# Kernel tuning notes

Hardware: AMD Instinct MI355X
Metric: run time of the kernel (lower is better)

## Reference

```python
import jax, jax.numpy as jnp
import numpy as np

N, E = 20000, 320000
DIMS = [(200, 64), (64, 128), (128, 256), (256, 256), (256, 512)]


def _embed(v):
    # NeRF positional encoding, multires=10, include_input, log-sampled freqs, [sin, cos] per freq
    freqs = 2.0 ** jnp.arange(10, dtype=jnp.float32)
    ang = v[:, None, :] * freqs[None, :, None]           # [N, 10, 3]
    sc = jnp.stack([jnp.sin(ang), jnp.cos(ang)], 2)      # [N, 10, 2, 3] (freq-major, sin then cos)
    return jnp.concatenate([v, sc.reshape(v.shape[0], -1)], -1)  # [N, 63]


def _edge_conv(h, src, dst, w1, b1, w2, b2):
    # PyG EdgeConv: nn([x_i, x_j - x_i]) aggregated by mean onto target i
    hi = h[dst]
    hj = h[src]
    m = jnp.concatenate([hi, hj - hi], -1)               # [E, 2*in]
    m = jax.nn.relu(m @ w1 + b1) @ w2 + b2               # [E, out]
    s = jax.ops.segment_sum(m, dst, num_segments=N)
    cnt = jax.ops.segment_sum(jnp.ones((m.shape[0], 1), m.dtype), dst, num_segments=N)
    return s / jnp.maximum(cnt, 1.0)                     # scatter-mean (0 for isolated nodes)


def _bn(h, g, b):
    # training-mode BatchNorm1d over nodes (biased variance, eps=1e-5)
    mu = h.mean(0)
    var = ((h - mu) ** 2).mean(0)
    return g * (h - mu) * jax.lax.rsqrt(var + 1e-5) + b


def setup_inputs() -> dict:
    key = jax.random.key(0)
    keys = iter(jax.random.split(key, 64))
    inp = {
        "x": jax.random.normal(next(keys), (N, 20), jnp.float32),
        "edge_index": jax.random.randint(next(keys), (2, E), 0, N, jnp.int32),
        "batch": jnp.zeros((N,), jnp.int32),
    }
    for i, (din, dout) in enumerate(DIMS, 1):
        inp[f"gc{i}_w1"] = jax.random.normal(next(keys), (2 * din, dout), jnp.float32) / np.sqrt(2.0 * din)
        inp[f"gc{i}_b1"] = jnp.zeros((dout,), jnp.float32)
        inp[f"gc{i}_w2"] = jax.random.normal(next(keys), (dout, dout), jnp.float32) / np.sqrt(1.0 * dout)
        inp[f"gc{i}_b2"] = jnp.zeros((dout,), jnp.float32)
    for i, d in enumerate([64, 128, 256, 256], 1):
        inp[f"n{i}_g"] = jnp.ones((d,), jnp.float32)
        inp[f"n{i}_b"] = jnp.zeros((d,), jnp.float32)
    return inp


def reference(x, edge_index, batch,
              gc1_w1, gc1_b1, gc1_w2, gc1_b2,
              gc2_w1, gc2_b1, gc2_w2, gc2_b2,
              gc3_w1, gc3_b1, gc3_w2, gc3_b2,
              gc4_w1, gc4_b1, gc4_w2, gc4_b2,
              gc5_w1, gc5_b1, gc5_w2, gc5_b2,
              n1_g, n1_b, n2_g, n2_b, n3_g, n3_b, n4_g, n4_b):
    src, dst = edge_index[0], edge_index[1]
    h = jnp.concatenate(
        [_embed(x[:, 0:3]), _embed(x[:, 3:6]), _embed(x[:, 6:9]), x[:, 9:20]], -1)  # [N, 200]
    h = jax.nn.relu(_bn(_edge_conv(h, src, dst, gc1_w1, gc1_b1, gc1_w2, gc1_b2), n1_g, n1_b))
    h = jax.nn.relu(_bn(_edge_conv(h, src, dst, gc2_w1, gc2_b1, gc2_w2, gc2_b2), n2_g, n2_b))
    h = jax.nn.relu(_bn(_edge_conv(h, src, dst, gc3_w1, gc3_b1, gc3_w2, gc3_b2), n3_g, n3_b))
    h = jax.nn.relu(_bn(_edge_conv(h, src, dst, gc4_w1, gc4_b1, gc4_w2, gc4_b2), n4_g, n4_b))
    return _edge_conv(h, src, dst, gc5_w1, gc5_b1, gc5_w2, gc5_b2)  # [N, 512]
```

## Files before the change

### kernel.cpp

```cpp
#include <hip/hip_runtime.h>
#include <math.h>

#define NNODES 20000
#define NEDGES 320000
#define NB 79

typedef __bf16 bf16x8 __attribute__((ext_vector_type(8)));
typedef float f32x4 __attribute__((ext_vector_type(4)));
typedef unsigned short u16x8 __attribute__((ext_vector_type(8)));

__device__ inline unsigned short f2bf(float x) {
  union { float f; unsigned int u; } q;
  q.f = x;
  unsigned int u = q.u;
  unsigned int r = (u + 0x7fffu + ((u >> 16) & 1u)) >> 16;
  return (unsigned short)r;
}

__device__ inline float bf2f(unsigned short u) {
  union { unsigned int u; float f; } q;
  q.u = ((unsigned int)u) << 16;
  return q.f;
}

__global__ __launch_bounds__(256) void embed_kernel(const float* __restrict__ x,
                                                    unsigned short* __restrict__ h) {
  int n = blockIdx.x * blockDim.x + threadIdx.x;
  if (n >= NNODES) return;
  const float* xr = x + (size_t)n * 20;
  unsigned short* hr = h + (size_t)n * 224;
#pragma unroll
  for (int g = 0; g < 3; ++g) {
    float v0 = xr[g * 3 + 0], v1 = xr[g * 3 + 1], v2 = xr[g * 3 + 2];
    unsigned short* o = hr + g * 63;
    o[0] = f2bf(v0); o[1] = f2bf(v1); o[2] = f2bf(v2);
    float f = 1.0f;
    for (int fr = 0; fr < 10; ++fr) {
      float s0, c0, s1, c1, s2, c2;
      sincosf(v0 * f, &s0, &c0);
      sincosf(v1 * f, &s1, &c1);
      sincosf(v2 * f, &s2, &c2);
      int base = 3 + fr * 6;
      o[base + 0] = f2bf(s0); o[base + 1] = f2bf(s1); o[base + 2] = f2bf(s2);
      o[base + 3] = f2bf(c0); o[base + 4] = f2bf(c1); o[base + 5] = f2bf(c2);
      f *= 2.0f;
    }
  }
  for (int j = 0; j < 11; ++j) hr[189 + j] = f2bf(xr[9 + j]);
  for (int j = 200; j < 224; ++j) hr[j] = 0;
}

__global__ __launch_bounds__(256) void count_kernel(const int* __restrict__ edst,
                                                    int* __restrict__ cnt) {
  int e = blockIdx.x * blockDim.x + threadIdx.x;
  if (e < NEDGES) atomicAdd(&cnt[edst[e]], 1);
}

__global__ __launch_bounds__(256) void scan_pass1(const int* __restrict__ cnt,
                                                  int* __restrict__ bsum) {
  __shared__ int red[256];
  int i = blockIdx.x * 256 + threadIdx.x;
  int v = (i < NNODES) ? cnt[i] : 0;
  red[threadIdx.x] = v;
  __syncthreads();
#pragma unroll
  for (int off = 128; off > 0; off >>= 1) {
    if (threadIdx.x < off) red[threadIdx.x] += red[threadIdx.x + off];
    __syncthreads();
  }
  if (threadIdx.x == 0) bsum[blockIdx.x] = red[0];
}

__global__ __launch_bounds__(128) void scan_pass2(const int* __restrict__ bsum,
                                                  int* __restrict__ boff) {
  __shared__ int buf[128];
  int t = threadIdx.x;
  int v = (t < NB) ? bsum[t] : 0;
  buf[t] = v;
  __syncthreads();
#pragma unroll
  for (int off = 1; off < 128; off <<= 1) {
    int u = (t >= off) ? buf[t - off] : 0;
    __syncthreads();
    buf[t] += u;
    __syncthreads();
  }
  if (t < NB) boff[t] = buf[t] - v;
}

__global__ __launch_bounds__(256) void scan_pass3(const int* __restrict__ cnt,
                                                  const int* __restrict__ boff,
                                                  int* __restrict__ rowptr,
                                                  int* __restrict__ head) {
  __shared__ int buf[256];
  int i = blockIdx.x * 256 + threadIdx.x;
  int v = (i < NNODES) ? cnt[i] : 0;
  buf[threadIdx.x] = v;
  __syncthreads();
#pragma unroll
  for (int off = 1; off < 256; off <<= 1) {
    int u = (threadIdx.x >= off) ? buf[threadIdx.x - off] : 0;
    __syncthreads();
    buf[threadIdx.x] += u;
    __syncthreads();
  }
  if (i < NNODES) {
    int excl = boff[blockIdx.x] + buf[threadIdx.x] - v;
    rowptr[i] = excl;
    head[i] = excl;
  }
  if (i == 0) rowptr[NNODES] = NEDGES;
}

__global__ __launch_bounds__(256) void scatter_kernel(const int* __restrict__ esrc,
                                                      const int* __restrict__ edst,
                                                      int* __restrict__ head,
                                                      int* __restrict__ csr_src) {
  int e = blockIdx.x * blockDim.x + threadIdx.x;
  if (e < NEDGES) {
    int pos = atomicAdd(&head[edst[e]], 1);
    csr_src[pos] = esrc[e];
  }
}

struct WPtrs {
  const float* w1[5];
  const float* w2[5];
};

#define WT1_TOTAL 503808
#define WT2_TOTAL 413696

__global__ __launch_bounds__(256) void weight_prep_kernel(
    WPtrs p, unsigned short* __restrict__ Wt1All,
    unsigned short* __restrict__ Wt2All) {
  int idx = blockIdx.x * 256 + threadIdx.x;
  if (idx < WT1_TOTAL) {
    int L, off, din, dout, Kpad;
    if (idx < 28672)       { L = 0; off = 0;      din = 200; dout = 64;  Kpad = 224; }
    else if (idx < 45056)  { L = 1; off = 28672;  din = 64;  dout = 128; Kpad = 64;  }
    else if (idx < 110592) { L = 2; off = 45056;  din = 128; dout = 256; Kpad = 128; }
    else if (idx < 241664) { L = 3; off = 110592; din = 256; dout = 256; Kpad = 256; }
    else                   { L = 4; off = 241664; din = 256; dout = 512; Kpad = 256; }
    int local = idx - off;
    int c = local / Kpad, k = local % Kpad;
    float v = 0.f;
    if (k < din)
      v = (c < dout) ? p.w1[L][(size_t)k * dout + c]
                     : p.w1[L][(size_t)(din + k) * dout + (c - dout)];
    Wt1All[idx] = f2bf(v);
    return;
  }
  int jdx = idx - WT1_TOTAL;
  if (jdx >= WT2_TOTAL) return;
  int L, off, d;
  if (jdx < 4096)        { L = 0; off = 0;      d = 64;  }
  else if (jdx < 20480)  { L = 1; off = 4096;   d = 128; }
  else if (jdx < 86016)  { L = 2; off = 20480;  d = 256; }
  else if (jdx < 151552) { L = 3; off = 86016;  d = 256; }
  else                   { L = 4; off = 151552; d = 512; }
  int local = jdx - off;
  int n = local / d, k = local % d;
  Wt2All[jdx] = f2bf(p.w2[L][(size_t)k * d + n]);
}

template <int EPI>
__global__ __launch_bounds__(256) void mfma_gemm_kernel(
    const unsigned short* __restrict__ A, int lda, int K,
    const unsigned short* __restrict__ Bt, int Ncol, int dhalf,
    const float* __restrict__ bias, const int* __restrict__ cnt,
    float* __restrict__ stats, void* __restrict__ Cout) {
  __shared__ unsigned short sA[128 * 40];
  __shared__ unsigned short sB[64 * 40];
  int tid = threadIdx.x;
  int bR = blockIdx.y * 128, bC = blockIdx.x * 64;
  int wid = tid >> 6, lane = tid & 63;
  int wr = wid >> 1, wc = wid & 1;
  int lr = lane & 15, lg = lane >> 4;

  f32x4 acc[4][2];
#pragma unroll
  for (int fr = 0; fr < 4; ++fr)
#pragma unroll
    for (int fc = 0; fc < 2; ++fc) acc[fr][fc] = f32x4{0.f, 0.f, 0.f, 0.f};

  for (int k0 = 0; k0 < K; k0 += 32) {
#pragma unroll
    for (int rep = 0; rep < 2; ++rep) {
      int idx = tid + rep * 256;
      int row = idx >> 2, kq = (idx & 3) * 8;
      int gr = bR + row;
      bf16x8 v;
      if (gr < NNODES) {
        v = *(const bf16x8*)(A + (size_t)gr * lda + k0 + kq);
      } else {
#pragma unroll
        for (int i = 0; i < 8; ++i) v[i] = (__bf16)0.f;
      }
      *(bf16x8*)(sA + row * 40 + kq) = v;
    }
    {
      int n = tid >> 2, kq = (tid & 3) * 8;
      bf16x8 v = *(const bf16x8*)(Bt + (size_t)(bC + n) * K + k0 + kq);
      *(bf16x8*)(sB + n * 40 + kq) = v;
    }
    __syncthreads();
    bf16x8 aF[4], bF[2];
#pragma unroll
    for (int fr = 0; fr < 4; ++fr)
      aF[fr] = *(const bf16x8*)(sA + (wr * 64 + fr * 16 + lr) * 40 + lg * 8);
#pragma unroll
    for (int fc = 0; fc < 2; ++fc)
      bF[fc] = *(const bf16x8*)(sB + (wc * 32 + fc * 16 + lr) * 40 + lg * 8);
#pragma unroll
    for (int fr = 0; fr < 4; ++fr)
#pragma unroll
      for (int fc = 0; fc < 2; ++fc)
        acc[fr][fc] = __builtin_amdgcn_mfma_f32_16x16x32_bf16(
            aF[fr], bF[fc], acc[fr][fc], 0, 0, 0);
    __syncthreads();
  }

  float csum[2] = {0.f, 0.f}, csum2[2] = {0.f, 0.f};
#pragma unroll
  for (int fr = 0; fr < 4; ++fr) {
#pragma unroll
    for (int j = 0; j < 4; ++j) {
      int gr = bR + wr * 64 + fr * 16 + lg * 4 + j;
      if (gr >= NNODES) continue;
      int ct = (EPI >= 1) ? cnt[gr] : 1;
#pragma unroll
      for (int fc = 0; fc < 2; ++fc) {
        int gc = bC + wc * 32 + fc * 16 + lr;
        float v = acc[fr][fc][j];
        if (EPI == 0) {
          if (gc < dhalf) v += bias[gc];
          ((unsigned short*)Cout)[(size_t)gr * Ncol + gc] = f2bf(v);
        } else {
          v = (ct > 0) ? (v + bias[gc]) : 0.f;
          ((float*)Cout)[(size_t)gr * Ncol + gc] = v;
          if (EPI == 2) {
            csum[fc] += v;
            csum2[fc] += v * v;
          }
        }
      }
    }
  }
  if (EPI == 2) {
#pragma unroll
    for (int fc = 0; fc < 2; ++fc) {
      float s = csum[fc], s2 = csum2[fc];
      s += __shfl_xor(s, 16, 64);
      s += __shfl_xor(s, 32, 64);
      s2 += __shfl_xor(s2, 16, 64);
      s2 += __shfl_xor(s2, 32, 64);
      if (lg == 0) {
        int gc = bC + wc * 32 + fc * 16 + lr;
        atomicAdd(&stats[gc], s);
        atomicAdd(&stats[Ncol + gc], s2);
      }
    }
  }
}

template <int D, int SLICES>
__global__ __launch_bounds__(256) void edge_agg_kernel(
    const unsigned short* __restrict__ AV, const int* __restrict__ rowptr,
    const int* __restrict__ csr_src, unsigned short* __restrict__ Y) {
  int slice = blockIdx.x % SLICES;
  int ngrp = blockIdx.x / SLICES;
  int tid = threadIdx.x;
  int ln = tid & 7;
  int sn = tid >> 3;
  int node = ngrp * 32 + sn;
  if (node >= NNODES) return;
  int c = slice * 64 + ln * 8;
  const unsigned short* Arow = AV + (size_t)node * 2 * D;
  u16x8 a8 = *(const u16x8*)(Arow + c);
  u16x8 v8 = *(const u16x8*)(Arow + D + c);
  float ad[8], acc[8];
#pragma unroll
  for (int i = 0; i < 8; ++i) {
    ad[i] = bf2f(a8[i]) - bf2f(v8[i]);
    acc[i] = 0.f;
  }
  int e0 = rowptr[node], e1 = rowptr[node + 1];
  int e = e0;
  for (; e + 3 < e1; e += 4) {
    int s0 = csr_src[e], s1 = csr_src[e + 1];
    int s2 = csr_src[e + 2], s3 = csr_src[e + 3];
    u16x8 w0 = *(const u16x8*)(AV + (size_t)s0 * 2 * D + D + c);
    u16x8 w1 = *(const u16x8*)(AV + (size_t)s1 * 2 * D + D + c);
    u16x8 w2 = *(const u16x8*)(AV + (size_t)s2 * 2 * D + D + c);
    u16x8 w3 = *(const u16x8*)(AV + (size_t)s3 * 2 * D + D + c);
#pragma unroll
    for (int i = 0; i < 8; ++i) {
      acc[i] += fmaxf(ad[i] + bf2f(w0[i]), 0.f) + fmaxf(ad[i] + bf2f(w1[i]), 0.f) +
                fmaxf(ad[i] + bf2f(w2[i]), 0.f) + fmaxf(ad[i] + bf2f(w3[i]), 0.f);
    }
  }
  for (; e < e1; ++e) {
    int s0 = csr_src[e];
    u16x8 w0 = *(const u16x8*)(AV + (size_t)s0 * 2 * D + D + c);
#pragma unroll
    for (int i = 0; i < 8; ++i) acc[i] += fmaxf(ad[i] + bf2f(w0[i]), 0.f);
  }
  float inv = (e1 > e0) ? 1.f / (float)(e1 - e0) : 0.f;
  u16x8 o;
#pragma unroll
  for (int i = 0; i < 8; ++i) o[i] = f2bf(acc[i] * inv);
  *(u16x8*)(Y + (size_t)node * D + c) = o;
}

__global__ __launch_bounds__(256) void bn_relu_kernel(
    const float* __restrict__ S, const float* __restrict__ stats,
    const float* __restrict__ g, const float* __restrict__ bb, int dout,
    unsigned short* __restrict__ Hout) {
  size_t idx = (size_t)blockIdx.x * blockDim.x + threadIdx.x;
  size_t total = (size_t)NNODES * dout;
  if (idx >= total) return;
  int c = (int)(idx % dout);
  float mu = stats[c] * (1.0f / NNODES);
  float var = stats[dout + c] * (1.0f / NNODES) - mu * mu;
  float y = S[idx];
  float v = g[c] * (y - mu) * rsqrtf(var + 1e-5f) + bb[c];
  Hout[idx] = f2bf(fmaxf(v, 0.f));
}

static void launch_edge_agg(int dout, const unsigned short* AV, const int* rowptr,
                            const int* csr_src, unsigned short* Y,
                            hipStream_t st) {
  const int NG = (NNODES + 31) / 32;
  switch (dout) {
    case 64:
      hipLaunchKernelGGL((edge_agg_kernel<64, 1>), dim3(NG * 1), dim3(256), 0, st,
                         AV, rowptr, csr_src, Y);
      break;
    case 128:
      hipLaunchKernelGGL((edge_agg_kernel<128, 2>), dim3(NG * 2), dim3(256), 0, st,
                         AV, rowptr, csr_src, Y);
      break;
    case 256:
      hipLaunchKernelGGL((edge_agg_kernel<256, 4>), dim3(NG * 4), dim3(256), 0, st,
                         AV, rowptr, csr_src, Y);
      break;
    case 512:
      hipLaunchKernelGGL((edge_agg_kernel<512, 8>), dim3(NG * 8), dim3(256), 0, st,
                         AV, rowptr, csr_src, Y);
      break;
  }
}

extern "C" void kernel_launch(void* const* d_in, const int* in_sizes, int n_in,
                              void* d_out, int out_size, void* d_ws,
                              size_t ws_size, hipStream_t stream) {
  const float* x = (const float*)d_in[0];
  const int* edge_index = (const int*)d_in[1];
  const int* esrc = edge_index;
  const int* edst = edge_index + NEDGES;

  const float* gw1[5] = {(const float*)d_in[3],  (const float*)d_in[7],
                         (const float*)d_in[11], (const float*)d_in[15],
                         (const float*)d_in[19]};
  const float* gb1[5] = {(const float*)d_in[4],  (const float*)d_in[8],
                         (const float*)d_in[12], (const float*)d_in[16],
                         (const float*)d_in[20]};
  const float* gw2[5] = {(const float*)d_in[5],  (const float*)d_in[9],
                         (const float*)d_in[13], (const float*)d_in[17],
                         (const float*)d_in[21]};
  const float* gb2[5] = {(const float*)d_in[6],  (const float*)d_in[10],
                         (const float*)d_in[14], (const float*)d_in[18],
                         (const float*)d_in[22]};
  const float* ng[4] = {(const float*)d_in[23], (const float*)d_in[25],
                        (const float*)d_in[27], (const float*)d_in[29]};
  const float* nb[4] = {(const float*)d_in[24], (const float*)d_in[26],
                        (const float*)d_in[28], (const float*)d_in[30]};

  unsigned short* AV = (unsigned short*)d_ws;
  float* S = (float*)(AV + (size_t)NNODES * 1024);
  unsigned short* Hbf = (unsigned short*)(S + (size_t)NNODES * 256);
  unsigned short* Ybf = Hbf + (size_t)NNODES * 256;
  unsigned short* Wt1All = Ybf + (size_t)NNODES * 512;
  unsigned short* Wt2All = Wt1All + WT1_TOTAL;
  int* cnt = (int*)(Wt2All + WT2_TOTAL);
  int* rowptr = cnt + NNODES;
  int* head = rowptr + NNODES + 1;
  int* csr_src = head + NNODES;
  int* bsum = csr_src + NEDGES;
  int* boff = bsum + NB;
  float* stats = (float*)(boff + NB);

  const int Kpads[5] = {224, 64, 128, 256, 256};
  const int douts[5] = {64, 128, 256, 256, 512};
  const int wt1_off[5] = {0, 28672, 45056, 110592, 241664};
  const int wt2_off[5] = {0, 4096, 20480, 86016, 151552};
  const int MBLK = (NNODES + 127) / 128;

  hipMemsetAsync(cnt, 0, NNODES * sizeof(int), stream);
  hipMemsetAsync(stats, 0, 4 * 1024 * sizeof(float), stream);
  count_kernel<<<(NEDGES + 255) / 256, 256, 0, stream>>>(edst, cnt);
  scan_pass1<<<NB, 256, 0, stream>>>(cnt, bsum);
  scan_pass2<<<1, 128, 0, stream>>>(bsum, boff);
  scan_pass3<<<NB, 256, 0, stream>>>(cnt, boff, rowptr, head);
  scatter_kernel<<<(NEDGES + 255) / 256, 256, 0, stream>>>(esrc, edst, head, csr_src);
  embed_kernel<<<(NNODES + 255) / 256, 256, 0, stream>>>(x, Hbf);

  WPtrs wp;
  for (int i = 0; i < 5; ++i) { wp.w1[i] = gw1[i]; wp.w2[i] = gw2[i]; }
  weight_prep_kernel<<<(WT1_TOTAL + WT2_TOTAL + 255) / 256, 256, 0, stream>>>(
      wp, Wt1All, Wt2All);

  int lda = 224;
  for (int L = 0; L < 5; ++L) {
    int Kp = Kpads[L], dout = douts[L];
    dim3 g1(2 * dout / 64, MBLK);
    hipLaunchKernelGGL((mfma_gemm_kernel<0>), g1, dim3(256), 0, stream,
                       Hbf, lda, Kp, Wt1All + wt1_off[L], 2 * dout, dout, gb1[L],
                       (const int*)nullptr, (float*)nullptr, (void*)AV);
    launch_edge_agg(dout, AV, rowptr, csr_src, Ybf, stream);
    dim3 g2(dout / 64, MBLK);
    if (L < 4) {
      float* lstats = stats + L * 1024;
      hipLaunchKernelGGL((mfma_gemm_kernel<2>), g2, dim3(256), 0, stream,
                         Ybf, dout, dout, Wt2All + wt2_off[L], dout, dout, gb2[L],
                         cnt, lstats, (void*)S);
      size_t total = (size_t)NNODES * dout;
      bn_relu_kernel<<<(total + 255) / 256, 256, 0, stream>>>(
          S, lstats, ng[L], nb[L], dout, Hbf);
      lda = dout;
    } else {
      hipLaunchKernelGGL((mfma_gemm_kernel<1>), g2, dim3(256), 0, stream,
                         Ybf, dout, dout, Wt2All + wt2_off[L], dout, dout, gb2[L],
                         cnt, (float*)nullptr, (void*)d_out);
    }
  }
}
```

Measured before the change: 461.7 us.

## Fuse BatchNorm+ReLU into next GEMM prologue and enlarge GEMM tiles to 128x128

The standalone bn_relu kernel is removed. The next layer's first GEMM now reads the fp32 pre-BN activations, builds per-channel scale and shift from the accumulated stats, and applies normalize+ReLU while loading the A tile into shared memory. The GEMM tile grows from 128x64 with K-step 32 to 128x128 with K-step 64, and layer-1 input padding goes from 224 to 256 so K divides the tile. This saves one full read/write pass of the hidden state per layer and improves reuse per block, at the cost of reading fp32 instead of bf16 A operands and fewer blocks in the grid.

```diff
diff --git a/kernel.cpp b/kernel.cpp
--- a/kernel.cpp
+++ b/kernel.cpp
@@ -28,7 +28,7 @@
   int n = blockIdx.x * blockDim.x + threadIdx.x;
   if (n >= NNODES) return;
   const float* xr = x + (size_t)n * 20;
-  unsigned short* hr = h + (size_t)n * 224;
+  unsigned short* hr = h + (size_t)n * 256;
 #pragma unroll
   for (int g = 0; g < 3; ++g) {
     float v0 = xr[g * 3 + 0], v1 = xr[g * 3 + 1], v2 = xr[g * 3 + 2];
@@ -47,7 +47,7 @@
     }
   }
   for (int j = 0; j < 11; ++j) hr[189 + j] = f2bf(xr[9 + j]);
-  for (int j = 200; j < 224; ++j) hr[j] = 0;
+  for (int j = 200; j < 256; ++j) hr[j] = 0;
 }
 
 __global__ __launch_bounds__(256) void count_kernel(const int* __restrict__ edst,
@@ -128,7 +128,7 @@
   const float* w2[5];
 };
 
-#define WT1_TOTAL 503808
+#define WT1_TOTAL 507904
 #define WT2_TOTAL 413696
 
 __global__ __launch_bounds__(256) void weight_prep_kernel(
@@ -137,11 +137,11 @@
   int idx = blockIdx.x * 256 + threadIdx.x;
   if (idx < WT1_TOTAL) {
     int L, off, din, dout, Kpad;
-    if (idx < 28672)       { L = 0; off = 0;      din = 200; dout = 64;  Kpad = 224; }
-    else if (idx < 45056)  { L = 1; off = 28672;  din = 64;  dout = 128; Kpad = 64;  }
-    else if (idx < 110592) { L = 2; off = 45056;  din = 128; dout = 256; Kpad = 128; }
-    else if (idx < 241664) { L = 3; off = 110592; din = 256; dout = 256; Kpad = 256; }
-    else                   { L = 4; off = 241664; din = 256; dout = 512; Kpad = 256; }
+    if (idx < 32768)       { L = 0; off = 0;      din = 200; dout = 64;  Kpad = 256; }
+    else if (idx < 49152)  { L = 1; off = 32768;  din = 64;  dout = 128; Kpad = 64;  }
+    else if (idx < 114688) { L = 2; off = 49152;  din = 128; dout = 256; Kpad = 128; }
+    else if (idx < 245760) { L = 3; off = 114688; din = 256; dout = 256; Kpad = 256; }
+    else                   { L = 4; off = 245760; din = 256; dout = 512; Kpad = 256; }
     int local = idx - off;
     int c = local / Kpad, k = local % Kpad;
     float v = 0.f;
@@ -164,64 +164,103 @@
   Wt2All[jdx] = f2bf(p.w2[L][(size_t)k * d + n]);
 }
 
-template <int EPI>
-__global__ __launch_bounds__(256) void mfma_gemm_kernel(
-    const unsigned short* __restrict__ A, int lda, int K,
+template <int EPI, int EPIA>
+__global__ __launch_bounds__(256) void gemm128_kernel(
+    const void* __restrict__ Aptr, int lda, int K,
     const unsigned short* __restrict__ Bt, int Ncol, int dhalf,
     const float* __restrict__ bias, const int* __restrict__ cnt,
-    float* __restrict__ stats, void* __restrict__ Cout) {
-  __shared__ unsigned short sA[128 * 40];
-  __shared__ unsigned short sB[64 * 40];
+    const float* __restrict__ pstats, const float* __restrict__ pg,
+    const float* __restrict__ pb, float* __restrict__ stats,
+    void* __restrict__ Cout) {
+  __shared__ unsigned short sA[128 * 72];
+  __shared__ unsigned short sB[128 * 72];
+  __shared__ float sScale[256], sShift[256];
   int tid = threadIdx.x;
-  int bR = blockIdx.y * 128, bC = blockIdx.x * 64;
+  int bR = blockIdx.y * 128, bC = blockIdx.x * 128;
   int wid = tid >> 6, lane = tid & 63;
   int wr = wid >> 1, wc = wid & 1;
   int lr = lane & 15, lg = lane >> 4;
 
-  f32x4 acc[4][2];
+  if (EPIA == 1) {
+    for (int c = tid; c < K; c += 256) {
+      float mu = pstats[c] * (1.0f / NNODES);
+      float var = pstats[K + c] * (1.0f / NNODES) - mu * mu;
+      float sc = pg[c] * rsqrtf(var + 1e-5f);
+      sScale[c] = sc;
+      sShift[c] = pb[c] - mu * sc;
+    }
+    __syncthreads();
+  }
+
+  f32x4 acc[4][4];
 #pragma unroll
   for (int fr = 0; fr < 4; ++fr)
 #pragma unroll
-    for (int fc = 0; fc < 2; ++fc) acc[fr][fc] = f32x4{0.f, 0.f, 0.f, 0.f};
-
-  for (int k0 = 0; k0 < K; k0 += 32) {
-#pragma unroll
-    for (int rep = 0; rep < 2; ++rep) {
-      int idx = tid + rep * 256;
-      int row = idx >> 2, kq = (idx & 3) * 8;
+    for (int fc = 0; fc < 4; ++fc) acc[fr][fc] = f32x4{0.f, 0.f, 0.f, 0.f};
+
+  for (int k0 = 0; k0 < K; k0 += 64) {
+#pragma unroll
+    for (int i = 0; i < 4; ++i) {
+      int idx = tid + i * 256;
+      int row = idx >> 3, c8 = (idx & 7) * 8;
       int gr = bR + row;
-      bf16x8 v;
-      if (gr < NNODES) {
-        v = *(const bf16x8*)(A + (size_t)gr * lda + k0 + kq);
+      if (EPIA == 0) {
+        bf16x8 v;
+        if (gr < NNODES) {
+          v = *(const bf16x8*)((const unsigned short*)Aptr + (size_t)gr * lda + k0 + c8);
+        } else {
+#pragma unroll
+          for (int j = 0; j < 8; ++j) v[j] = (__bf16)0.f;
+        }
+        *(bf16x8*)(sA + row * 72 + c8) = v;
       } else {
-#pragma unroll
-        for (int i = 0; i < 8; ++i) v[i] = (__bf16)0.f;
+        const float* Af = (const float*)Aptr;
+        float uv[8];
+#pragma unroll
+        for (int j = 0; j < 8; ++j) uv[j] = 0.f;
+        if (gr < NNODES) {
+          float4 u0 = *(const float4*)(Af + (size_t)gr * lda + k0 + c8);
+          float4 u1 = *(const float4*)(Af + (size_t)gr * lda + k0 + c8 + 4);
+          uv[0] = u0.x; uv[1] = u0.y; uv[2] = u0.z; uv[3] = u0.w;
+          uv[4] = u1.x; uv[5] = u1.y; uv[6] = u1.z; uv[7] = u1.w;
+        }
+        u16x8 o;
+#pragma unroll
+        for (int j = 0; j < 8; ++j) {
+          int k = k0 + c8 + j;
+          o[j] = f2bf(fmaxf(uv[j] * sScale[k] + sShift[k], 0.f));
+        }
+        *(u16x8*)(sA + row * 72 + c8) = o;
       }
-      *(bf16x8*)(sA + row * 40 + kq) = v;
-    }
-    {
-      int n = tid >> 2, kq = (tid & 3) * 8;
-      bf16x8 v = *(const bf16x8*)(Bt + (size_t)(bC + n) * K + k0 + kq);
-      *(bf16x8*)(sB + n * 40 + kq) = v;
-    }
-    __syncthreads();
-    bf16x8 aF[4], bF[2];
-#pragma unroll
-    for (int fr = 0; fr < 4; ++fr)
-      aF[fr] = *(const bf16x8*)(sA + (wr * 64 + fr * 16 + lr) * 40 + lg * 8);
-#pragma unroll
-    for (int fc = 0; fc < 2; ++fc)
-      bF[fc] = *(const bf16x8*)(sB + (wc * 32 + fc * 16 + lr) * 40 + lg * 8);
-#pragma unroll
-    for (int fr = 0; fr < 4; ++fr)
-#pragma unroll
-      for (int fc = 0; fc < 2; ++fc)
-        acc[fr][fc] = __builtin_amdgcn_mfma_f32_16x16x32_bf16(
-            aF[fr], bF[fc], acc[fr][fc], 0, 0, 0);
-    __syncthreads();
-  }
-
-  float csum[2] = {0.f, 0.f}, csum2[2] = {0.f, 0.f};
+    }
+#pragma unroll
+    for (int i = 0; i < 4; ++i) {
+      int idx = tid + i * 256;
+      int n = idx >> 3, c8 = (idx & 7) * 8;
+      bf16x8 v = *(const bf16x8*)(Bt + (size_t)(bC + n) * K + k0 + c8);
+      *(bf16x8*)(sB + n * 72 + c8) = v;
+    }
+    __syncthreads();
+#pragma unroll
+    for (int ks = 0; ks < 2; ++ks) {
+      bf16x8 aF[4], bF[4];
+#pragma unroll
+      for (int fr = 0; fr < 4; ++fr)
+        aF[fr] = *(const bf16x8*)(sA + (wr * 64 + fr * 16 + lr) * 72 + ks * 32 + lg * 8);
+#pragma unroll
+      for (int fc = 0; fc < 4; ++fc)
+        bF[fc] = *(const bf16x8*)(sB + (wc * 64 + fc * 16 + lr) * 72 + ks * 32 + lg * 8);
+#pragma unroll
+      for (int fr = 0; fr < 4; ++fr)
+#pragma unroll
+        for (int fc = 0; fc < 4; ++fc)
+          acc[fr][fc] = __builtin_amdgcn_mfma_f32_16x16x32_bf16(
+              aF[fr], bF[fc], acc[fr][fc], 0, 0, 0);
+    }
+    __syncthreads();
+  }
+
+  float csum[4] = {0.f, 0.f, 0.f, 0.f}, csum2[4] = {0.f, 0.f, 0.f, 0.f};
 #pragma unroll
   for (int fr = 0; fr < 4; ++fr) {
 #pragma unroll
@@ -230,8 +269,8 @@
       if (gr >= NNODES) continue;
       int ct = (EPI >= 1) ? cnt[gr] : 1;
 #pragma unroll
-      for (int fc = 0; fc < 2; ++fc) {
-        int gc = bC + wc * 32 + fc * 16 + lr;
+      for (int fc = 0; fc < 4; ++fc) {
+        int gc = bC + wc * 64 + fc * 16 + lr;
         float v = acc[fr][fc][j];
         if (EPI == 0) {
           if (gc < dhalf) v += bias[gc];
@@ -249,17 +288,107 @@
   }
   if (EPI == 2) {
 #pragma unroll
-    for (int fc = 0; fc < 2; ++fc) {
+    for (int fc = 0; fc < 4; ++fc) {
       float s = csum[fc], s2 = csum2[fc];
       s += __shfl_xor(s, 16, 64);
       s += __shfl_xor(s, 32, 64);
       s2 += __shfl_xor(s2, 16, 64);
       s2 += __shfl_xor(s2, 32, 64);
       if (lg == 0) {
-        int gc = bC + wc * 32 + fc * 16 + lr;
+        int gc = bC + wc * 64 + fc * 16 + lr;
         atomicAdd(&stats[gc], s);
         atomicAdd(&stats[Ncol + gc], s2);
       }
+    }
+  }
+}
+
+__global__ __launch_bounds__(256) void gemm64_stats_kernel(
+    const unsigned short* __restrict__ A, int lda, int K,
+    const unsigned short* __restrict__ Bt, int Ncol,
+    const float* __restrict__ bias, const int* __restrict__ cnt,
+    float* __restrict__ stats, float* __restrict__ Cout) {
+  __shared__ unsigned short sA[128 * 40];
+  __shared__ unsigned short sB[64 * 40];
+  int tid = threadIdx.x;
+  int bR = blockIdx.y * 128, bC = blockIdx.x * 64;
+  int wid = tid >> 6, lane = tid & 63;
+  int wr = wid >> 1, wc = wid & 1;
+  int lr = lane & 15, lg = lane >> 4;
+
+  f32x4 acc[4][2];
+#pragma unroll
+  for (int fr = 0; fr < 4; ++fr)
+#pragma unroll
+    for (int fc = 0; fc < 2; ++fc) acc[fr][fc] = f32x4{0.f, 0.f, 0.f, 0.f};
+
+  for (int k0 = 0; k0 < K; k0 += 32) {
+#pragma unroll
+    for (int rep = 0; rep < 2; ++rep) {
+      int idx = tid + rep * 256;
+      int row = idx >> 2, kq = (idx & 3) * 8;
+      int gr = bR + row;
+      bf16x8 v;
+      if (gr < NNODES) {
+        v = *(const bf16x8*)(A + (size_t)gr * lda + k0 + kq);
+      } else {
+#pragma unroll
+        for (int i = 0; i < 8; ++i) v[i] = (__bf16)0.f;
+      }
+      *(bf16x8*)(sA + row * 40 + kq) = v;
+    }
+    {
+      int n = tid >> 2, kq = (tid & 3) * 8;
+      bf16x8 v = *(const bf16x8*)(Bt + (size_t)(bC + n) * K + k0 + kq);
+      *(bf16x8*)(sB + n * 40 + kq) = v;
+    }
+    __syncthreads();
+    bf16x8 aF[4], bF[2];
+#pragma unroll
+    for (int fr = 0; fr < 4; ++fr)
+      aF[fr] = *(const bf16x8*)(sA + (wr * 64 + fr * 16 + lr) * 40 + lg * 8);
+#pragma unroll
+    for (int fc = 0; fc < 2; ++fc)
+      bF[fc] = *(const bf16x8*)(sB + (wc * 32 + fc * 16 + lr) * 40 + lg * 8);
+#pragma unroll
+    for (int fr = 0; fr < 4; ++fr)
+#pragma unroll
+      for (int fc = 0; fc < 2; ++fc)
+        acc[fr][fc] = __builtin_amdgcn_mfma_f32_16x16x32_bf16(
+            aF[fr], bF[fc], acc[fr][fc], 0, 0, 0);
+    __syncthreads();
+  }
+
+  float csum[2] = {0.f, 0.f}, csum2[2] = {0.f, 0.f};
+#pragma unroll
+  for (int fr = 0; fr < 4; ++fr) {
+#pragma unroll
+    for (int j = 0; j < 4; ++j) {
+      int gr = bR + wr * 64 + fr * 16 + lg * 4 + j;
+      if (gr >= NNODES) continue;
+      int ct = cnt[gr];
+#pragma unroll
+      for (int fc = 0; fc < 2; ++fc) {
+        int gc = bC + wc * 32 + fc * 16 + lr;
+        float v = acc[fr][fc][j];
+        v = (ct > 0) ? (v + bias[gc]) : 0.f;
+        Cout[(size_t)gr * Ncol + gc] = v;
+        csum[fc] += v;
+        csum2[fc] += v * v;
+      }
+    }
+  }
+#pragma unroll
+  for (int fc = 0; fc < 2; ++fc) {
+    float s = csum[fc], s2 = csum2[fc];
+    s += __shfl_xor(s, 16, 64);
+    s += __shfl_xor(s, 32, 64);
+    s2 += __shfl_xor(s2, 16, 64);
+    s2 += __shfl_xor(s2, 32, 64);
+    if (lg == 0) {
+      int gc = bC + wc * 32 + fc * 16 + lr;
+      atomicAdd(&stats[gc], s);
+      atomicAdd(&stats[Ncol + gc], s2);
     }
   }
 }
@@ -311,21 +440,6 @@
 #pragma unroll
   for (int i = 0; i < 8; ++i) o[i] = f2bf(acc[i] * inv);
   *(u16x8*)(Y + (size_t)node * D + c) = o;
-}
-
-__global__ __launch_bounds__(256) void bn_relu_kernel(
-    const float* __restrict__ S, const float* __restrict__ stats,
-    const float* __restrict__ g, const float* __restrict__ bb, int dout,
-    unsigned short* __restrict__ Hout) {
-  size_t idx = (size_t)blockIdx.x * blockDim.x + threadIdx.x;
-  size_t total = (size_t)NNODES * dout;
-  if (idx >= total) return;
-  int c = (int)(idx % dout);
-  float mu = stats[c] * (1.0f / NNODES);
-  float var = stats[dout + c] * (1.0f / NNODES) - mu * mu;
-  float y = S[idx];
-  float v = g[c] * (y - mu) * rsqrtf(var + 1e-5f) + bb[c];
-  Hout[idx] = f2bf(fmaxf(v, 0.f));
 }
 
 static void launch_edge_agg(int dout, const unsigned short* AV, const int* rowptr,
@@ -391,9 +505,9 @@
   int* boff = bsum + NB;
   float* stats = (float*)(boff + NB);
 
-  const int Kpads[5] = {224, 64, 128, 256, 256};
+  const int Kpads[5] = {256, 64, 128, 256, 256};
   const int douts[5] = {64, 128, 256, 256, 512};
-  const int wt1_off[5] = {0, 28672, 45056, 110592, 241664};
+  const int wt1_off[5] = {0, 32768, 49152, 114688, 245760};
   const int wt2_off[5] = {0, 4096, 20480, 86016, 151552};
   const int MBLK = (NNODES + 127) / 128;
 
@@ -411,28 +525,42 @@
   weight_prep_kernel<<<(WT1_TOTAL + WT2_TOTAL + 255) / 256, 256, 0, stream>>>(
       wp, Wt1All, Wt2All);
 
-  int lda = 224;
   for (int L = 0; L < 5; ++L) {
     int Kp = Kpads[L], dout = douts[L];
-    dim3 g1(2 * dout / 64, MBLK);
-    hipLaunchKernelGGL((mfma_gemm_kernel<0>), g1, dim3(256), 0, stream,
-                       Hbf, lda, Kp, Wt1All + wt1_off[L], 2 * dout, dout, gb1[L],
-                       (const int*)nullptr, (float*)nullptr, (void*)AV);
+    dim3 g1(2 * dout / 128, MBLK);
+    if (L == 0) {
+      hipLaunchKernelGGL((gemm128_kernel<0, 0>), g1, dim3(256), 0, stream,
+                         (const void*)Hbf, 256, Kp, Wt1All + wt1_off[L], 2 * dout,
+                         dout, gb1[L], (const int*)nullptr, (const float*)nullptr,
+                         (const float*)nullptr, (const float*)nullptr,
+                         (float*)nullptr, (void*)AV);
+    } else {
+      hipLaunchKernelGGL((gemm128_kernel<0, 1>), g1, dim3(256), 0, stream,
+                         (const void*)S, Kp, Kp, Wt1All + wt1_off[L], 2 * dout,
+                         dout, gb1[L], (const int*)nullptr,
+                         stats + (L - 1) * 1024, ng[L - 1], nb[L - 1],
+                         (float*)nullptr, (void*)AV);
+    }
     launch_edge_agg(dout, AV, rowptr, csr_src, Ybf, stream);
-    dim3 g2(dout / 64, MBLK);
-    if (L < 4) {
-      float* lstats = stats + L * 1024;
-      hipLaunchKernelGGL((mfma_gemm_kernel<2>), g2, dim3(256), 0, stream,
-                         Ybf, dout, dout, Wt2All + wt2_off[L], dout, dout, gb2[L],
-                         cnt, lstats, (void*)S);
-      size_t total = (size_t)NNODES * dout;
-      bn_relu_kernel<<<(total + 255) / 256, 256, 0, stream>>>(
-          S, lstats, ng[L], nb[L], dout, Hbf);
-      lda = dout;
+    if (L == 0) {
+      dim3 g2(1, MBLK);
+      gemm64_stats_kernel<<<g2, 256, 0, stream>>>(
+          Ybf, dout, dout, Wt2All + wt2_off[L], dout, gb2[L], cnt,
+          stats + L * 1024, S);
+    } else if (L < 4) {
+      dim3 g2(dout / 128, MBLK);
+      hipLaunchKernelGGL((gemm128_kernel<2, 0>), g2, dim3(256), 0, stream,
+                         (const void*)Ybf, dout, dout, Wt2All + wt2_off[L], dout,
+                         dout, gb2[L], cnt, (const float*)nullptr,
+                         (const float*)nullptr, (const float*)nullptr,
+                         stats + L * 1024, (void*)S);
     } else {
-      hipLaunchKernelGGL((mfma_gemm_kernel<1>), g2, dim3(256), 0, stream,
-                         Ybf, dout, dout, Wt2All + wt2_off[L], dout, dout, gb2[L],
-                         cnt, (float*)nullptr, (void*)d_out);
-    }
-  }
-}
+      dim3 g2(dout / 128, MBLK);
+      hipLaunchKernelGGL((gemm128_kernel<1, 0>), g2, dim3(256), 0, stream,
+                         (const void*)Ybf, dout, dout, Wt2All + wt2_off[L], dout,
+                         dout, gb2[L], cnt, (const float*)nullptr,
+                         (const float*)nullptr, (const float*)nullptr,
+                         (float*)nullptr, (void*)d_out);
+    }
+  }
+}
```

Result: slower. 482.6 us (+4.5%).
